# Optimization experiments

Measured on AMD Instinct MI355X. Metric: run time of the kernel, lower is better.

The kernel has to match this reference:

```python
import jax, jax.numpy as jnp
import numpy as np
import math

EMBED = 1024
HEADS = 16
HEAD_DIM = EMBED // HEADS
B, S = 2, 2048


def setup_inputs() -> dict:
    key = jax.random.key(0)
    ks = jax.random.split(key, 12)
    sc = 1.0 / math.sqrt(EMBED)
    inp = {
        'query': jax.random.normal(ks[0], (B, S, EMBED), jnp.float32),
        'key': jax.random.normal(ks[1], (B, S, EMBED), jnp.float32),
        'values': jax.random.normal(ks[2], (B, S, EMBED), jnp.float32),
        # causal mask, broadcastable to [B, H, S, S]; masked where == 0
        'mask': jnp.tril(jnp.ones((S, S), jnp.int32))[None, None, :, :],
        'Wq': jax.random.normal(ks[3], (EMBED, EMBED), jnp.float32) * sc,
        'bq': jnp.zeros((EMBED,), jnp.float32),
        'Wk': jax.random.normal(ks[4], (EMBED, EMBED), jnp.float32) * sc,
        'bk': jnp.zeros((EMBED,), jnp.float32),
        'Wv': jax.random.normal(ks[5], (EMBED, EMBED), jnp.float32) * sc,
        'bv': jnp.zeros((EMBED,), jnp.float32),
        'Wo': jax.random.normal(ks[6], (EMBED, EMBED), jnp.float32) * sc,
        'bo': jnp.zeros((EMBED,), jnp.float32),
    }
    return inp


def reference(query, key, values, mask, Wq, bq, Wk, bk, Wv, bv, Wo, bo):
    # linear projections (torch Linear: x @ W.T + b)
    q = query @ Wq.T + bq
    k = key @ Wk.T + bk
    v = values @ Wv.T + bv
    b, sq, _ = q.shape
    sk = k.shape[1]
    q = q.reshape(b, sq, HEADS, HEAD_DIM)  # bqhd
    k = k.reshape(b, sk, HEADS, HEAD_DIM)  # bkhd
    v = v.reshape(b, sk, HEADS, HEAD_DIM)  # bkhd
    energy = jnp.einsum('bqhd,bkhd->bhqk', q, k) / math.sqrt(HEAD_DIM)
    energy = jnp.where(mask == 0, jnp.float32(-1e10), energy)
    attn = jax.nn.softmax(energy, axis=-1)
    out = jnp.einsum('bhqk,bkhd->bqhd', attn, v).reshape(b, sq, EMBED)
    return out @ Wo.T + bo
```

## Files before the change

### kernel.cpp

```cpp
#include <hip/hip_runtime.h>

typedef unsigned short u16;
typedef unsigned int   u32;
typedef __attribute__((ext_vector_type(4))) float f32x4;
typedef __attribute__((ext_vector_type(8))) short bf16x8;
typedef __attribute__((ext_vector_type(4))) u32   u32x4;
typedef __attribute__((ext_vector_type(4))) u16   u16x4;

#define AS1 __attribute__((address_space(1)))
#define AS3 __attribute__((address_space(3)))

__device__ __forceinline__ u16 f2bf(float f) {
  union { float f; u32 u; } v; v.f = f;
  u32 r = v.u + 0x7FFFu + ((v.u >> 16) & 1u);
  return (u16)(r >> 16);
}

__device__ __forceinline__ void g2l16(const void* g, void* l) {
  __builtin_amdgcn_global_load_lds((const AS1 u32*)g, (AS3 u32*)l, 16, 0, 0);
}

struct CvtArgs {
  const float* src[7];
  u16*         dst[7];
  int          n4[7];
};

__global__ __launch_bounds__(256) void cvt_kernel(CvtArgs a) {
  const int ai = blockIdx.y;
  const f32x4* s = (const f32x4*)a.src[ai];
  u16x4*       d = (u16x4*)a.dst[ai];
  const int n4 = a.n4[ai];
  for (int i = blockIdx.x * 256 + threadIdx.x; i < n4; i += gridDim.x * 256) {
    f32x4 v = s[i];
    u16x4 o;
    o[0] = f2bf(v[0]); o[1] = f2bf(v[1]); o[2] = f2bf(v[2]); o[3] = f2bf(v[3]);
    d[i] = o;
  }
}

template <typename OutT, int TM>
__device__ __forceinline__ void gemm_core(
    const u16* __restrict__ A, const u16* __restrict__ W,
    const float* __restrict__ bias, bool rowbias,
    OutT* __restrict__ C, int ldc, int row0, int col0,
    u16* sA, u16* sB, int tid)
{
  constexpr int K = 1024;
  constexpr int MF = TM / 32;
  const int lane = tid & 63, wid = tid >> 6;
  const int l15 = lane & 15, hi = lane >> 4;
  const int wr = (wid >> 1) * (TM / 2), wc = (wid & 1) * 64;

  f32x4 acc[MF][4];
#pragma unroll
  for (int i = 0; i < MF; ++i)
#pragma unroll
    for (int j = 0; j < 4; ++j) acc[i][j] = f32x4{0.f, 0.f, 0.f, 0.f};

  auto stage = [&](int kt) {
#pragma unroll
    for (int it = 0; it < TM / 64; ++it) {
      int idx = it * 256 + tid;
      int r = idx >> 2, g = idx & 3;
      int gs = g ^ ((r >> 1) & 3);
      g2l16(A + (size_t)(row0 + r) * K + kt * 32 + gs * 8, sA + idx * 8);
    }
#pragma unroll
    for (int it = 0; it < 2; ++it) {
      int idx = it * 256 + tid;
      int r = idx >> 2, g = idx & 3;
      int gs = g ^ ((r >> 1) & 3);
      g2l16(W + (size_t)(col0 + r) * K + kt * 32 + gs * 8, sB + idx * 8);
    }
  };

  stage(0);
  for (int kt = 0; kt < K / 32; ++kt) {
    __syncthreads();
    bf16x8 aF[MF], bF[4];
#pragma unroll
    for (int mf = 0; mf < MF; ++mf) {
      int r = wr + mf * 16 + l15;
      int g = hi ^ ((r >> 1) & 3);
      aF[mf] = *(const bf16x8*)(sA + r * 32 + g * 8);
    }
#pragma unroll
    for (int nf = 0; nf < 4; ++nf) {
      int r = wc + nf * 16 + l15;
      int g = hi ^ ((r >> 1) & 3);
      bF[nf] = *(const bf16x8*)(sB + r * 32 + g * 8);
    }
#pragma unroll
    for (int mf = 0; mf < MF; ++mf)
#pragma unroll
      for (int nf = 0; nf < 4; ++nf)
        acc[mf][nf] = __builtin_amdgcn_mfma_f32_16x16x32_bf16(aF[mf], bF[nf], acc[mf][nf], 0, 0, 0);
    __syncthreads();
    if (kt + 1 < K / 32) stage(kt + 1);
  }

#pragma unroll
  for (int nf = 0; nf < 4; ++nf) {
    int gcol = col0 + wc + nf * 16 + l15;
    float bcol = rowbias ? 0.f : bias[gcol];
#pragma unroll
    for (int mf = 0; mf < MF; ++mf) {
#pragma unroll
      for (int r = 0; r < 4; ++r) {
        int grow = row0 + wr + mf * 16 + hi * 4 + r;
        float bv = rowbias ? bias[grow] : bcol;
        float v = acc[mf][nf][r] + bv;
        if constexpr (sizeof(OutT) == 2) {
          ((u16*)C)[(size_t)grow * ldc + gcol] = f2bf(v);
        } else {
          ((float*)C)[(size_t)grow * ldc + gcol] = v;
        }
      }
    }
  }
}

struct ProjArgs {
  const u16* A[3]; const u16* W[3]; const float* bias[3];
  u16* C[3];
};

__global__ __launch_bounds__(256, 2) void gemm_proj(ProjArgs p) {
  __shared__ alignas(16) u16 sA[128 * 32];
  __shared__ alignas(16) u16 sB[128 * 32];
  const int bid = blockIdx.x;
  int which, row0, col0, ldc;
  bool rowbias;
  if (bid < 512) {
    which = bid >> 8;
    int l = bid & 255;
    col0 = (l & 7) << 7;
    row0 = (l >> 3) << 7;
    ldc = 1024; rowbias = false;
  } else {
    which = 2;
    int l = bid - 512;
    col0 = (l & 31) << 7;
    row0 = (l >> 5) << 7;
    ldc = 4096; rowbias = true;
  }
  gemm_core<u16, 128>(p.A[which], p.W[which], p.bias[which], rowbias,
                      p.C[which], ldc, row0, col0, sA, sB, threadIdx.x);
}

__global__ __launch_bounds__(256, 2) void gemm_out(
    const u16* __restrict__ A, const u16* __restrict__ W,
    const float* __restrict__ bias, float* __restrict__ C)
{
  __shared__ alignas(16) u16 sA[64 * 32];
  __shared__ alignas(16) u16 sB[128 * 32];
  const int bid = blockIdx.x;
  const int col0 = (bid & 7) << 7;
  const int row0 = (bid >> 3) << 6;
  gemm_core<float, 64>(A, W, bias, false, C, 1024, row0, col0, sA, sB, threadIdx.x);
}

__global__ __launch_bounds__(256, 4) void attn_fwd(
    const u16* __restrict__ Q, const u16* __restrict__ Kg, const u16* __restrict__ VT,
    u16* __restrict__ ctx)
{
  __shared__ alignas(16) u16 sK[2][64 * 64];
  __shared__ alignas(16) u16 sVt[2][64 * 64];
  __shared__ alignas(16) u16 sP[4][16 * 64];

  const int tid = threadIdx.x;
  const int lane = tid & 63, wid = tid >> 6;
  const int l15 = lane & 15, hi = lane >> 4;

  const int wg = blockIdx.x;
  const int jj = wg >> 5, bh = wg & 31;
  const int rr = jj >> 3, kk = jj & 7;
  int xt;
  if (rr == 0)      xt = 31 - kk;
  else if (rr == 1) xt = 16 + kk;
  else if (rr == 2) xt = 15 - kk;
  else              xt = kk;

  const int b = bh >> 4, h = bh & 15;
  const int q0 = xt * 64;
  const int q0w = q0 + wid * 16;
  const size_t base  = ((size_t)b * 2048) * 1024 + h * 64;
  const size_t vbase = (size_t)(h * 64) * 4096 + b * 2048;

  bf16x8 qf[2];
#pragma unroll
  for (int kh = 0; kh < 2; ++kh)
    qf[kh] = *(const bf16x8*)(Q + base + (size_t)(q0w + l15) * 1024 + kh * 32 + hi * 8);

  f32x4 o[4];
  float lS[4];
#pragma unroll
  for (int nf = 0; nf < 4; ++nf) o[nf] = f32x4{0.f, 0.f, 0.f, 0.f};
#pragma unroll
  for (int r = 0; r < 4; ++r) lS[r] = 0.f;

  u16* sPw = &sP[wid][0];
  const int nt = xt + 1;

  auto issueK = [&](int ti, int bb) {
#pragma unroll
    for (int it = 0; it < 2; ++it) {
      int idx = it * 256 + tid;
      int r = idx >> 3, g = idx & 7;
      int gs = g ^ (r & 7);
      g2l16(Kg + base + (size_t)(ti * 64 + r) * 1024 + gs * 8, &sK[bb][idx * 8]);
    }
  };
  auto issueV = [&](int ti, int bb) {
#pragma unroll
    for (int it = 0; it < 2; ++it) {
      int idx = it * 256 + tid;
      int r = idx >> 3, g = idx & 7;
      int gs = g ^ (r & 7);
      g2l16(VT + vbase + (size_t)r * 4096 + ti * 64 + gs * 8, &sVt[bb][idx * 8]);
    }
  };

  issueK(0, 0);
  issueV(0, 0);
  __syncthreads();

  constexpr float SCL = 0.125f * 1.44269504f;

  for (int ti = 0; ti < nt; ++ti) {
    const int cur = ti & 1;
    const bool pf = (ti + 1 < nt);
    if (pf) {
      issueK(ti + 1, cur ^ 1);
      issueV(ti + 1, cur ^ 1);
    }

    const int kv0 = ti * 64;
    const bool needmask = (ti == xt);
    const u16* sKc = &sK[cur][0];
    const u16* sVc = &sVt[cur][0];

    f32x4 s[4];
#pragma unroll
    for (int n = 0; n < 4; ++n) s[n] = f32x4{0.f, 0.f, 0.f, 0.f};
#pragma unroll
    for (int n = 0; n < 4; ++n) {
      int kvr = n * 16 + l15;
      bf16x8 kf0 = *(const bf16x8*)(sKc + kvr * 64 + ((hi) ^ (kvr & 7)) * 8);
      bf16x8 kf1 = *(const bf16x8*)(sKc + kvr * 64 + ((4 + hi) ^ (kvr & 7)) * 8);
      s[n] = __builtin_amdgcn_mfma_f32_16x16x32_bf16(qf[0], kf0, s[n], 0, 0, 0);
      s[n] = __builtin_amdgcn_mfma_f32_16x16x32_bf16(qf[1], kf1, s[n], 0, 0, 0);
    }

#pragma unroll
    for (int r = 0; r < 4; ++r) {
      float lsum = 0.f;
#pragma unroll
      for (int n = 0; n < 4; ++n) {
        float sv = s[n][r] * SCL;
        if (needmask) {
          int qa = q0w + hi * 4 + r;
          int ka = kv0 + n * 16 + l15;
          if (ka > qa) sv = -1e30f;
        }
        float p = __builtin_amdgcn_exp2f(sv);
        s[n][r] = p;
        lsum += p;
      }
      lS[r] += lsum;
    }

#pragma unroll
    for (int n = 0; n < 4; ++n) {
      int c = n * 16 + l15;
#pragma unroll
      for (int r = 0; r < 4; ++r) {
        int q = hi * 4 + r;
        sPw[q * 64 + (c ^ ((q & 7) << 3))] = f2bf(s[n][r]);
      }
    }

#pragma unroll
    for (int kq = 0; kq < 2; ++kq) {
      bf16x8 pa, vb[4];
      pa = *(const bf16x8*)(sPw + l15 * 64 + ((kq * 32 + hi * 8) ^ ((l15 & 7) << 3)));
#pragma unroll
      for (int nf = 0; nf < 4; ++nf) {
        int rd = nf * 16 + l15;
        vb[nf] = *(const bf16x8*)(sVc + rd * 64 + ((kq * 4 + hi) ^ (rd & 7)) * 8);
      }
#pragma unroll
      for (int nf = 0; nf < 4; ++nf)
        o[nf] = __builtin_amdgcn_mfma_f32_16x16x32_bf16(pa, vb[nf], o[nf], 0, 0, 0);
    }

    __syncthreads();
  }

#pragma unroll
  for (int r = 0; r < 4; ++r) {
    float t = lS[r];
    t += __shfl_xor(t, 1);
    t += __shfl_xor(t, 2);
    t += __shfl_xor(t, 4);
    t += __shfl_xor(t, 8);
    float inv = 1.f / t;
    size_t rowoff = base + (size_t)(q0w + hi * 4 + r) * 1024;
#pragma unroll
    for (int nf = 0; nf < 4; ++nf)
      ctx[rowoff + nf * 16 + l15] = f2bf(o[nf][r] * inv);
  }
}

extern "C" void kernel_launch(void* const* d_in, const int* in_sizes, int n_in,
                              void* d_out, int out_size, void* d_ws, size_t ws_size,
                              hipStream_t stream) {
  const float* query = (const float*)d_in[0];
  const float* key   = (const float*)d_in[1];
  const float* vals  = (const float*)d_in[2];
  const float* Wq = (const float*)d_in[4];
  const float* bq = (const float*)d_in[5];
  const float* Wk = (const float*)d_in[6];
  const float* bk = (const float*)d_in[7];
  const float* Wv = (const float*)d_in[8];
  const float* bv = (const float*)d_in[9];
  const float* Wo = (const float*)d_in[10];
  const float* bo = (const float*)d_in[11];
  float* out = (float*)d_out;

  if (ws_size < 58720256) return;

  u16* ws = (u16*)d_ws;
  u16* xq = ws + 0;
  u16* xk = ws + 4194304;
  u16* xv = ws + 8388608;
  u16* wq = ws + 12582912;
  u16* wk = ws + 13631488;
  u16* wv = ws + 14680064;
  u16* wo = ws + 15728640;
  u16* Qb = ws + 16777216;
  u16* Kb = ws + 20971520;
  u16* VT = ws + 25165824;
  u16* ctx = xq;

  CvtArgs ca;
  ca.src[0] = query; ca.dst[0] = xq; ca.n4[0] = 1048576;
  ca.src[1] = key;   ca.dst[1] = xk; ca.n4[1] = 1048576;
  ca.src[2] = vals;  ca.dst[2] = xv; ca.n4[2] = 1048576;
  ca.src[3] = Wq;    ca.dst[3] = wq; ca.n4[3] = 262144;
  ca.src[4] = Wk;    ca.dst[4] = wk; ca.n4[4] = 262144;
  ca.src[5] = Wv;    ca.dst[5] = wv; ca.n4[5] = 262144;
  ca.src[6] = Wo;    ca.dst[6] = wo; ca.n4[6] = 262144;
  cvt_kernel<<<dim3(256, 7), 256, 0, stream>>>(ca);

  ProjArgs pa;
  pa.A[0] = xq; pa.W[0] = wq; pa.bias[0] = bq; pa.C[0] = Qb;
  pa.A[1] = xk; pa.W[1] = wk; pa.bias[1] = bk; pa.C[1] = Kb;
  pa.A[2] = wv; pa.W[2] = xv; pa.bias[2] = bv; pa.C[2] = VT;
  gemm_proj<<<dim3(768), 256, 0, stream>>>(pa);

  attn_fwd<<<dim3(1024), 256, 0, stream>>>(Qb, Kb, VT, ctx);

  gemm_out<<<dim3(512), 256, 0, stream>>>(ctx, wo, bo, out);
}
```

Measured before the change: 119.8 us.

## Use 32x32 MFMA attention with 128-row query tiles and deeper GEMM K-tiles

The attention kernel now gives each block 128 query rows, with 32 rows per wave. It switches to 32x32x16 MFMA, which halves the grid and lets each K/V tile loaded into shared memory serve more query rows. The GEMMs stage a K depth of 64 per step instead of 32, issue the next stage before the MFMAs, and remap block ids so neighbouring blocks spread across XCDs. The aim is fewer barriers and less global traffic per FLOP. In exchange it uses more registers and LDS, which lowers occupancy, and the causal work per block is less balanced.

```diff
diff --git a/kernel.cpp b/kernel.cpp
--- a/kernel.cpp
+++ b/kernel.cpp
@@ -2,10 +2,11 @@
 
 typedef unsigned short u16;
 typedef unsigned int   u32;
-typedef __attribute__((ext_vector_type(4))) float f32x4;
-typedef __attribute__((ext_vector_type(8))) short bf16x8;
-typedef __attribute__((ext_vector_type(4))) u32   u32x4;
-typedef __attribute__((ext_vector_type(4))) u16   u16x4;
+typedef __attribute__((ext_vector_type(4)))  float f32x4;
+typedef __attribute__((ext_vector_type(16))) float f32x16;
+typedef __attribute__((ext_vector_type(8)))  short bf16x8;
+typedef __attribute__((ext_vector_type(4)))  u32   u32x4;
+typedef __attribute__((ext_vector_type(4)))  u16   u16x4;
 
 #define AS1 __attribute__((address_space(1)))
 #define AS3 __attribute__((address_space(3)))
@@ -40,7 +41,7 @@
 }
 
 template <typename OutT, int TM>
-__device__ __forceinline__ void gemm_core(
+__device__ __forceinline__ void gemm_core64(
     const u16* __restrict__ A, const u16* __restrict__ W,
     const float* __restrict__ bias, bool rowbias,
     OutT* __restrict__ C, int ldc, int row0, int col0,
@@ -60,44 +61,48 @@
 
   auto stage = [&](int kt) {
 #pragma unroll
-    for (int it = 0; it < TM / 64; ++it) {
+    for (int it = 0; it < TM / 32; ++it) {
       int idx = it * 256 + tid;
-      int r = idx >> 2, g = idx & 3;
-      int gs = g ^ ((r >> 1) & 3);
-      g2l16(A + (size_t)(row0 + r) * K + kt * 32 + gs * 8, sA + idx * 8);
-    }
-#pragma unroll
-    for (int it = 0; it < 2; ++it) {
+      int r = idx >> 3, g = idx & 7;
+      int gs = g ^ (r & 7);
+      g2l16(A + (size_t)(row0 + r) * K + kt * 64 + gs * 8, sA + idx * 8);
+    }
+#pragma unroll
+    for (int it = 0; it < 4; ++it) {
       int idx = it * 256 + tid;
-      int r = idx >> 2, g = idx & 3;
-      int gs = g ^ ((r >> 1) & 3);
-      g2l16(W + (size_t)(col0 + r) * K + kt * 32 + gs * 8, sB + idx * 8);
+      int r = idx >> 3, g = idx & 7;
+      int gs = g ^ (r & 7);
+      g2l16(W + (size_t)(col0 + r) * K + kt * 64 + gs * 8, sB + idx * 8);
     }
   };
 
   stage(0);
-  for (int kt = 0; kt < K / 32; ++kt) {
+  for (int kt = 0; kt < K / 64; ++kt) {
     __syncthreads();
-    bf16x8 aF[MF], bF[4];
+    bf16x8 aF[MF][2], bF[4][2];
 #pragma unroll
     for (int mf = 0; mf < MF; ++mf) {
       int r = wr + mf * 16 + l15;
-      int g = hi ^ ((r >> 1) & 3);
-      aF[mf] = *(const bf16x8*)(sA + r * 32 + g * 8);
+#pragma unroll
+      for (int kh = 0; kh < 2; ++kh)
+        aF[mf][kh] = *(const bf16x8*)(sA + r * 64 + ((kh * 4 + hi) ^ (r & 7)) * 8);
     }
 #pragma unroll
     for (int nf = 0; nf < 4; ++nf) {
       int r = wc + nf * 16 + l15;
-      int g = hi ^ ((r >> 1) & 3);
-      bF[nf] = *(const bf16x8*)(sB + r * 32 + g * 8);
-    }
-#pragma unroll
-    for (int mf = 0; mf < MF; ++mf)
-#pragma unroll
-      for (int nf = 0; nf < 4; ++nf)
-        acc[mf][nf] = __builtin_amdgcn_mfma_f32_16x16x32_bf16(aF[mf], bF[nf], acc[mf][nf], 0, 0, 0);
+#pragma unroll
+      for (int kh = 0; kh < 2; ++kh)
+        bF[nf][kh] = *(const bf16x8*)(sB + r * 64 + ((kh * 4 + hi) ^ (r & 7)) * 8);
+    }
     __syncthreads();
-    if (kt + 1 < K / 32) stage(kt + 1);
+    if (kt + 1 < K / 64) stage(kt + 1);
+#pragma unroll
+    for (int kh = 0; kh < 2; ++kh)
+#pragma unroll
+      for (int mf = 0; mf < MF; ++mf)
+#pragma unroll
+        for (int nf = 0; nf < 4; ++nf)
+          acc[mf][nf] = __builtin_amdgcn_mfma_f32_16x16x32_bf16(aF[mf][kh], bF[nf][kh], acc[mf][nf], 0, 0, 0);
   }
 
 #pragma unroll
@@ -127,81 +132,73 @@
 };
 
 __global__ __launch_bounds__(256, 2) void gemm_proj(ProjArgs p) {
-  __shared__ alignas(16) u16 sA[128 * 32];
-  __shared__ alignas(16) u16 sB[128 * 32];
-  const int bid = blockIdx.x;
+  __shared__ alignas(16) u16 sA[128 * 64];
+  __shared__ alignas(16) u16 sB[128 * 64];
+  const int w = (blockIdx.x & 7) * 96 + (blockIdx.x >> 3);
   int which, row0, col0, ldc;
   bool rowbias;
-  if (bid < 512) {
-    which = bid >> 8;
-    int l = bid & 255;
+  if (w < 512) {
+    which = w >> 8;
+    int l = w & 255;
     col0 = (l & 7) << 7;
     row0 = (l >> 3) << 7;
     ldc = 1024; rowbias = false;
   } else {
     which = 2;
-    int l = bid - 512;
+    int l = w - 512;
     col0 = (l & 31) << 7;
     row0 = (l >> 5) << 7;
     ldc = 4096; rowbias = true;
   }
-  gemm_core<u16, 128>(p.A[which], p.W[which], p.bias[which], rowbias,
-                      p.C[which], ldc, row0, col0, sA, sB, threadIdx.x);
+  gemm_core64<u16, 128>(p.A[which], p.W[which], p.bias[which], rowbias,
+                        p.C[which], ldc, row0, col0, sA, sB, threadIdx.x);
 }
 
 __global__ __launch_bounds__(256, 2) void gemm_out(
     const u16* __restrict__ A, const u16* __restrict__ W,
     const float* __restrict__ bias, float* __restrict__ C)
 {
-  __shared__ alignas(16) u16 sA[64 * 32];
-  __shared__ alignas(16) u16 sB[128 * 32];
-  const int bid = blockIdx.x;
-  const int col0 = (bid & 7) << 7;
-  const int row0 = (bid >> 3) << 6;
-  gemm_core<float, 64>(A, W, bias, false, C, 1024, row0, col0, sA, sB, threadIdx.x);
-}
-
-__global__ __launch_bounds__(256, 4) void attn_fwd(
+  __shared__ alignas(16) u16 sA[64 * 64];
+  __shared__ alignas(16) u16 sB[128 * 64];
+  const int w = (blockIdx.x & 7) * 64 + (blockIdx.x >> 3);
+  const int col0 = (w & 7) << 7;
+  const int row0 = (w >> 3) << 6;
+  gemm_core64<float, 64>(A, W, bias, false, C, 1024, row0, col0, sA, sB, threadIdx.x);
+}
+
+__global__ __launch_bounds__(256, 2) void attn_fwd(
     const u16* __restrict__ Q, const u16* __restrict__ Kg, const u16* __restrict__ VT,
     u16* __restrict__ ctx)
 {
   __shared__ alignas(16) u16 sK[2][64 * 64];
   __shared__ alignas(16) u16 sVt[2][64 * 64];
-  __shared__ alignas(16) u16 sP[4][16 * 64];
+  __shared__ alignas(16) u16 sP[4][32 * 64];
 
   const int tid = threadIdx.x;
   const int lane = tid & 63, wid = tid >> 6;
-  const int l15 = lane & 15, hi = lane >> 4;
-
-  const int wg = blockIdx.x;
-  const int jj = wg >> 5, bh = wg & 31;
-  const int rr = jj >> 3, kk = jj & 7;
-  int xt;
-  if (rr == 0)      xt = 31 - kk;
-  else if (rr == 1) xt = 16 + kk;
-  else if (rr == 2) xt = 15 - kk;
-  else              xt = kk;
-
+  const int l31 = lane & 31, h5 = lane >> 5;
+
+  const int bid = blockIdx.x;
+  const int j = bid >> 5, bh = bid & 31;
+  const int xt = (j < 8) ? (15 - j) : (j - 8);
   const int b = bh >> 4, h = bh & 15;
-  const int q0 = xt * 64;
-  const int q0w = q0 + wid * 16;
+  const int q0 = xt * 128;
+  const int q0w = q0 + wid * 32;
   const size_t base  = ((size_t)b * 2048) * 1024 + h * 64;
   const size_t vbase = (size_t)(h * 64) * 4096 + b * 2048;
 
-  bf16x8 qf[2];
-#pragma unroll
-  for (int kh = 0; kh < 2; ++kh)
-    qf[kh] = *(const bf16x8*)(Q + base + (size_t)(q0w + l15) * 1024 + kh * 32 + hi * 8);
-
-  f32x4 o[4];
-  float lS[4];
-#pragma unroll
-  for (int nf = 0; nf < 4; ++nf) o[nf] = f32x4{0.f, 0.f, 0.f, 0.f};
-#pragma unroll
-  for (int r = 0; r < 4; ++r) lS[r] = 0.f;
+  bf16x8 qa[4];
+#pragma unroll
+  for (int c = 0; c < 4; ++c)
+    qa[c] = *(const bf16x8*)(Q + base + (size_t)(q0w + l31) * 1024 + c * 16 + h5 * 8);
+
+  f32x16 o[2];
+  float lS[16];
+#pragma unroll
+  for (int e = 0; e < 16; ++e) { o[0][e] = 0.f; o[1][e] = 0.f; lS[e] = 0.f; }
 
   u16* sPw = &sP[wid][0];
-  const int nt = xt + 1;
+  const int nt = 2 * xt + 2;
 
   auto issueK = [&](int ti, int bb) {
 #pragma unroll
@@ -237,79 +234,82 @@
     }
 
     const int kv0 = ti * 64;
-    const bool needmask = (ti == xt);
     const u16* sKc = &sK[cur][0];
     const u16* sVc = &sVt[cur][0];
 
-    f32x4 s[4];
-#pragma unroll
-    for (int n = 0; n < 4; ++n) s[n] = f32x4{0.f, 0.f, 0.f, 0.f};
-#pragma unroll
-    for (int n = 0; n < 4; ++n) {
-      int kvr = n * 16 + l15;
-      bf16x8 kf0 = *(const bf16x8*)(sKc + kvr * 64 + ((hi) ^ (kvr & 7)) * 8);
-      bf16x8 kf1 = *(const bf16x8*)(sKc + kvr * 64 + ((4 + hi) ^ (kvr & 7)) * 8);
-      s[n] = __builtin_amdgcn_mfma_f32_16x16x32_bf16(qf[0], kf0, s[n], 0, 0, 0);
-      s[n] = __builtin_amdgcn_mfma_f32_16x16x32_bf16(qf[1], kf1, s[n], 0, 0, 0);
-    }
-
-#pragma unroll
-    for (int r = 0; r < 4; ++r) {
-      float lsum = 0.f;
-#pragma unroll
-      for (int n = 0; n < 4; ++n) {
-        float sv = s[n][r] * SCL;
-        if (needmask) {
-          int qa = q0w + hi * 4 + r;
-          int ka = kv0 + n * 16 + l15;
-          if (ka > qa) sv = -1e30f;
-        }
-        float p = __builtin_amdgcn_exp2f(sv);
-        s[n][r] = p;
-        lsum += p;
-      }
-      lS[r] += lsum;
-    }
-
-#pragma unroll
-    for (int n = 0; n < 4; ++n) {
-      int c = n * 16 + l15;
-#pragma unroll
-      for (int r = 0; r < 4; ++r) {
-        int q = hi * 4 + r;
-        sPw[q * 64 + (c ^ ((q & 7) << 3))] = f2bf(s[n][r]);
-      }
-    }
-
-#pragma unroll
-    for (int kq = 0; kq < 2; ++kq) {
-      bf16x8 pa, vb[4];
-      pa = *(const bf16x8*)(sPw + l15 * 64 + ((kq * 32 + hi * 8) ^ ((l15 & 7) << 3)));
-#pragma unroll
-      for (int nf = 0; nf < 4; ++nf) {
-        int rd = nf * 16 + l15;
-        vb[nf] = *(const bf16x8*)(sVc + rd * 64 + ((kq * 4 + hi) ^ (rd & 7)) * 8);
-      }
-#pragma unroll
-      for (int nf = 0; nf < 4; ++nf)
-        o[nf] = __builtin_amdgcn_mfma_f32_16x16x32_bf16(pa, vb[nf], o[nf], 0, 0, 0);
+    if (kv0 <= q0w + 31) {
+      const bool needmask = (kv0 + 63 > q0w);
+
+      f32x16 s[2];
+#pragma unroll
+      for (int e = 0; e < 16; ++e) { s[0][e] = 0.f; s[1][e] = 0.f; }
+#pragma unroll
+      for (int n = 0; n < 2; ++n) {
+        int row = n * 32 + l31;
+#pragma unroll
+        for (int c = 0; c < 4; ++c) {
+          bf16x8 kb = *(const bf16x8*)(sKc + row * 64 + (((c * 2 + h5) ^ (row & 7))) * 8);
+          s[n] = __builtin_amdgcn_mfma_f32_32x32x16_bf16(qa[c], kb, s[n], 0, 0, 0);
+        }
+      }
+
+#pragma unroll
+      for (int n = 0; n < 2; ++n) {
+        int ka = kv0 + n * 32 + l31;
+#pragma unroll
+        for (int r = 0; r < 16; ++r) {
+          float sv = s[n][r] * SCL;
+          if (needmask) {
+            int qrow = q0w + (r & 3) + 8 * (r >> 2) + 4 * h5;
+            if (ka > qrow) sv = -1e30f;
+          }
+          float p = __builtin_amdgcn_exp2f(sv);
+          s[n][r] = p;
+          lS[r] += p;
+        }
+      }
+
+#pragma unroll
+      for (int n = 0; n < 2; ++n) {
+        int kv = n * 32 + l31;
+#pragma unroll
+        for (int r = 0; r < 16; ++r) {
+          int q = (r & 3) + 8 * (r >> 2) + 4 * h5;
+          sPw[q * 64 + (kv ^ ((q & 7) << 3))] = f2bf(s[n][r]);
+        }
+      }
+
+      bf16x8 pa[4];
+#pragma unroll
+      for (int c = 0; c < 4; ++c)
+        pa[c] = *(const bf16x8*)(sPw + l31 * 64 + ((c * 16 + h5 * 8) ^ ((l31 & 7) << 3)));
+#pragma unroll
+      for (int nf = 0; nf < 2; ++nf) {
+        int d = nf * 32 + l31;
+#pragma unroll
+        for (int c = 0; c < 4; ++c) {
+          bf16x8 vb = *(const bf16x8*)(sVc + d * 64 + (((c * 2 + h5) ^ (d & 7))) * 8);
+          o[nf] = __builtin_amdgcn_mfma_f32_32x32x16_bf16(pa[c], vb, o[nf], 0, 0, 0);
+        }
+      }
     }
 
     __syncthreads();
   }
 
 #pragma unroll
-  for (int r = 0; r < 4; ++r) {
+  for (int r = 0; r < 16; ++r) {
     float t = lS[r];
     t += __shfl_xor(t, 1);
     t += __shfl_xor(t, 2);
     t += __shfl_xor(t, 4);
     t += __shfl_xor(t, 8);
+    t += __shfl_xor(t, 16);
     float inv = 1.f / t;
-    size_t rowoff = base + (size_t)(q0w + hi * 4 + r) * 1024;
-#pragma unroll
-    for (int nf = 0; nf < 4; ++nf)
-      ctx[rowoff + nf * 16 + l15] = f2bf(o[nf][r] * inv);
+    int q = (r & 3) + 8 * (r >> 2) + 4 * h5;
+    size_t rowoff = base + (size_t)(q0w + q) * 1024;
+    ctx[rowoff + l31]      = f2bf(o[0][r] * inv);
+    ctx[rowoff + 32 + l31] = f2bf(o[1][r] * inv);
   }
 }
 
@@ -360,7 +360,7 @@
   pa.A[2] = wv; pa.W[2] = xv; pa.bias[2] = bv; pa.C[2] = VT;
   gemm_proj<<<dim3(768), 256, 0, stream>>>(pa);
 
-  attn_fwd<<<dim3(1024), 256, 0, stream>>>(Qb, Kb, VT, ctx);
+  attn_fwd<<<dim3(512), 256, 0, stream>>>(Qb, Kb, VT, ctx);
 
   gemm_out<<<dim3(512), 256, 0, stream>>>(ctx, wo, bo, out);
 }
```

New measurement: 131.1 us. 1.09x slower.
